# Performance work log

Measured on AMD Instinct MI355X. Metric: run time of the kernel, lower is better.

Reference implementation:

```python
import jax, jax.numpy as jnp
import numpy as np

H = 16
D_MODEL = 1024
D_K = D_MODEL // H


def setup_inputs() -> dict:
    key = jax.random.key(0)
    ks = jax.random.split(key, 11)
    B, S = 4, 2048
    scale = 1.0 / np.sqrt(D_MODEL)
    inp = {
        "query": jax.random.normal(ks[0], (B, S, D_MODEL), dtype=jnp.float32),
        "key": jax.random.normal(ks[1], (B, S, D_MODEL), dtype=jnp.float32),
        "value": jax.random.normal(ks[2], (B, S, D_MODEL), dtype=jnp.float32),
        "Wq": jax.random.normal(ks[3], (D_MODEL, D_MODEL), dtype=jnp.float32) * scale,
        "bq": jnp.zeros((D_MODEL,), dtype=jnp.float32),
        "Wk": jax.random.normal(ks[4], (D_MODEL, D_MODEL), dtype=jnp.float32) * scale,
        "bk": jnp.zeros((D_MODEL,), dtype=jnp.float32),
        "Wv": jax.random.normal(ks[5], (D_MODEL, D_MODEL), dtype=jnp.float32) * scale,
        "bv": jnp.zeros((D_MODEL,), dtype=jnp.float32),
        "Wo": jax.random.normal(ks[6], (D_MODEL, D_MODEL), dtype=jnp.float32) * scale,
        "bo": jnp.zeros((D_MODEL,), dtype=jnp.float32),
    }
    return inp


def reference(query, key, value, Wq, bq, Wk, bk, Wv, bv, Wo, bo):
    B, S, _ = query.shape

    def proj(x, W, b):
        # nn.Linear: x @ W.T + b, then split heads -> [B, H, S, D_K]
        y = jnp.einsum("bsd,ed->bse", x, W) + b
        return y.reshape(B, S, H, D_K).transpose(0, 2, 1, 3)

    q = proj(query, Wq, bq)
    k = proj(key, Wk, bk)
    v = proj(value, Wv, bv)

    scores = jnp.einsum("bhqd,bhkd->bhqk", q, k) / jnp.sqrt(jnp.float32(D_K))
    attn = jax.nn.softmax(scores, axis=-1)
    out = jnp.einsum("bhqk,bhkd->bhqd", attn, v)  # [B,H,S,D_K]
    out = out.transpose(0, 2, 1, 3).reshape(B, S, H * D_K)
    # final linear (dropout disabled in eval / deterministic reference)
    return jnp.einsum("bsd,ed->bse", out, Wo) + bo
```

## Files before the change

### kernel.cpp

```cpp
#include <hip/hip_runtime.h>
#include <stdint.h>

typedef __attribute__((ext_vector_type(8))) short short8;
typedef __attribute__((ext_vector_type(4))) float floatx4;

#define DEV __device__ __forceinline__

DEV unsigned short f2bf(float x) {
  unsigned u = __float_as_uint(x);
  u += 0x7fffu + ((u >> 16) & 1u);
  return (unsigned short)(u >> 16);
}

DEV unsigned pkbf(float hi, float lo) {
  return __builtin_amdgcn_perm(__float_as_uint(hi) + 0x8000u,
                               __float_as_uint(lo) + 0x8000u, 0x07060302u);
}

DEV void load_lds16(const unsigned short* g, unsigned short* l) {
  __builtin_amdgcn_global_load_lds(
      (const __attribute__((address_space(1))) void*)g,
      (__attribute__((address_space(3))) void*)l, 16, 0, 0);
}

DEV void lds_fence() { asm volatile("" ::: "memory"); }

__global__ void cvt_all(const float* __restrict__ Wq, const float* __restrict__ Wk,
                        const float* __restrict__ Wv, const float* __restrict__ Wo,
                        const float* __restrict__ Xq, const float* __restrict__ Xk,
                        const float* __restrict__ Xv,
                        unsigned short* __restrict__ Wb, unsigned short* __restrict__ XqB,
                        unsigned short* __restrict__ XkB, unsigned short* __restrict__ XvB) {
  int bid = blockIdx.x;
  const float* src;
  unsigned short* dst;
  int off;
  if (bid < 4096) {
    int sel = bid >> 10;
    src = sel == 0 ? Wq : sel == 1 ? Wk : sel == 2 ? Wv : Wo;
    dst = Wb + (size_t)sel * 1048576;
    off = bid & 1023;
  } else {
    bid -= 4096;
    int sel = bid >> 13;
    src = sel == 0 ? Xq : sel == 1 ? Xk : Xv;
    dst = sel == 0 ? XqB : sel == 1 ? XkB : XvB;
    off = bid & 8191;
  }
  int i = (off * 256 + threadIdx.x) * 4;
  float4 v = *(const float4*)(src + i);
  uint2 o;
  o.x = pkbf(v.y, v.x);
  o.y = pkbf(v.w, v.z);
  *(uint2*)(dst + i) = o;
}

#define SCQ (0.125f * 1.44269504089f)
__global__ __launch_bounds__(256, 2) void qkv_gemm(
    const unsigned short* __restrict__ XqB, const unsigned short* __restrict__ XkB,
    const unsigned short* __restrict__ XvB,
    const unsigned short* __restrict__ Wb,
    const float* __restrict__ bq, const float* __restrict__ bk, const float* __restrict__ bv,
    unsigned short* __restrict__ Qp, unsigned short* __restrict__ Kp,
    unsigned short* __restrict__ VTp) {
  __shared__ alignas(16) unsigned short Xs[2][128 * 32];
  __shared__ alignas(16) unsigned short Ws[2][128 * 32];
  const int z = blockIdx.z;
  const unsigned short* X = z == 0 ? XqB : z == 1 ? XkB : XvB;
  const unsigned short* W = Wb + (size_t)z * 1048576;
  const float* bias = z == 0 ? bq : z == 1 ? bk : bv;

  const int tid = threadIdx.x;
  const int lane = tid & 63, wave = tid >> 6;
  const int lcol = lane & 15, quad = lane >> 4;
  const int wo = blockIdx.x * 128;
  const int xo = blockIdx.y * 128;
  const int wm = (wave & 1) * 64;
  const int wn = (wave >> 1) * 64;

  floatx4 acc[4][4];
  for (int mi = 0; mi < 4; ++mi)
    for (int ni = 0; ni < 4; ++ni)
      for (int r = 0; r < 4; ++r) acc[mi][ni][r] = 0.f;

  {
    int c = tid;
    load_lds16(W + (size_t)(wo + (c >> 2)) * 1024 + (c & 3) * 8, Ws[0] + c * 8);
    load_lds16(X + (size_t)(xo + (c >> 2)) * 1024 + (c & 3) * 8, Xs[0] + c * 8);
    c = tid + 256;
    load_lds16(W + (size_t)(wo + (c >> 2)) * 1024 + (c & 3) * 8, Ws[0] + c * 8);
    load_lds16(X + (size_t)(xo + (c >> 2)) * 1024 + (c & 3) * 8, Xs[0] + c * 8);
  }
  __syncthreads();

  for (int kt = 0; kt < 32; ++kt) {
    const int cur = kt & 1;
    if (kt != 31) {
      const int k0 = (kt + 1) * 32;
      int c = tid;
      load_lds16(W + (size_t)(wo + (c >> 2)) * 1024 + k0 + (c & 3) * 8, Ws[cur ^ 1] + c * 8);
      load_lds16(X + (size_t)(xo + (c >> 2)) * 1024 + k0 + (c & 3) * 8, Xs[cur ^ 1] + c * 8);
      c = tid + 256;
      load_lds16(W + (size_t)(wo + (c >> 2)) * 1024 + k0 + (c & 3) * 8, Ws[cur ^ 1] + c * 8);
      load_lds16(X + (size_t)(xo + (c >> 2)) * 1024 + k0 + (c & 3) * 8, Xs[cur ^ 1] + c * 8);
    }
    const unsigned short* Ab = (z < 2) ? Xs[cur] : Ws[cur];
    const unsigned short* Bb = (z < 2) ? Ws[cur] : Xs[cur];
    short8 af[4], bfr[4];
#pragma unroll
    for (int mi = 0; mi < 4; ++mi)
      af[mi] = *(const short8*)(Ab + (wm + mi * 16 + lcol) * 32 + quad * 8);
#pragma unroll
    for (int ni = 0; ni < 4; ++ni)
      bfr[ni] = *(const short8*)(Bb + (wn + ni * 16 + lcol) * 32 + quad * 8);
#pragma unroll
    for (int mi = 0; mi < 4; ++mi)
#pragma unroll
      for (int ni = 0; ni < 4; ++ni)
        acc[mi][ni] = __builtin_amdgcn_mfma_f32_16x16x32_bf16(af[mi], bfr[ni], acc[mi][ni], 0, 0, 0);
    __syncthreads();
  }

  if (z < 2) {
    unsigned short* Out = z == 0 ? Qp : Kp;
    const float scl = z == 0 ? SCQ : 1.f;
#pragma unroll
    for (int ni = 0; ni < 4; ++ni) {
      int col = wo + wn + ni * 16 + lcol;
      float bvx = bias[col];
      int h = col >> 6, d = col & 63;
#pragma unroll
      for (int mi = 0; mi < 4; ++mi) {
        int rbase = xo + wm + mi * 16 + quad * 4;
#pragma unroll
        for (int r = 0; r < 4; ++r) {
          int grow = rbase + r;
          int bb = grow >> 11, s = grow & 2047;
          Out[((size_t)(bb * 16 + h) * 2048 + s) * 64 + d] = f2bf((acc[mi][ni][r] + bvx) * scl);
        }
      }
    }
  } else {
#pragma unroll
    for (int mi = 0; mi < 4; ++mi) {
      int dbase = wo + wm + mi * 16 + quad * 4;
#pragma unroll
      for (int r = 0; r < 4; ++r) {
        int dg = dbase + r;
        float bvx = bias[dg];
        int h = dg >> 6, dk = dg & 63;
#pragma unroll
        for (int ni = 0; ni < 4; ++ni) {
          int sg = xo + wn + ni * 16 + lcol;
          int bb = sg >> 11, ss = sg & 2047;
          VTp[((size_t)(bb * 16 + h) * 64 + dk) * 2048 + ss] = f2bf(acc[mi][ni][r] + bvx);
        }
      }
    }
  }
}

__global__ __launch_bounds__(256, 2) void gemm_o(
    const unsigned short* __restrict__ A, const unsigned short* __restrict__ Bw,
    const float* __restrict__ bias, float* __restrict__ Out) {
  __shared__ alignas(16) unsigned short As[2][128 * 32];
  __shared__ alignas(16) unsigned short Bs[2][128 * 32];
  const int tid = threadIdx.x;
  const int lane = tid & 63, wave = tid >> 6;
  const int lcol = lane & 15, quad = lane >> 4;
  const int n0 = blockIdx.x * 128;
  const int m0 = blockIdx.y * 128;
  const int wm = (wave & 1) * 64;
  const int wn = (wave >> 1) * 64;

  floatx4 acc[4][4];
  for (int mi = 0; mi < 4; ++mi)
    for (int ni = 0; ni < 4; ++ni)
      for (int r = 0; r < 4; ++r) acc[mi][ni][r] = 0.f;

  {
    int c = tid;
    load_lds16(Bw + (size_t)(n0 + (c >> 2)) * 1024 + (c & 3) * 8, Bs[0] + c * 8);
    load_lds16(A  + (size_t)(m0 + (c >> 2)) * 1024 + (c & 3) * 8, As[0] + c * 8);
    c = tid + 256;
    load_lds16(Bw + (size_t)(n0 + (c >> 2)) * 1024 + (c & 3) * 8, Bs[0] + c * 8);
    load_lds16(A  + (size_t)(m0 + (c >> 2)) * 1024 + (c & 3) * 8, As[0] + c * 8);
  }
  __syncthreads();

  for (int kt = 0; kt < 32; ++kt) {
    const int cur = kt & 1;
    if (kt != 31) {
      const int k0 = (kt + 1) * 32;
      int c = tid;
      load_lds16(Bw + (size_t)(n0 + (c >> 2)) * 1024 + k0 + (c & 3) * 8, Bs[cur ^ 1] + c * 8);
      load_lds16(A  + (size_t)(m0 + (c >> 2)) * 1024 + k0 + (c & 3) * 8, As[cur ^ 1] + c * 8);
      c = tid + 256;
      load_lds16(Bw + (size_t)(n0 + (c >> 2)) * 1024 + k0 + (c & 3) * 8, Bs[cur ^ 1] + c * 8);
      load_lds16(A  + (size_t)(m0 + (c >> 2)) * 1024 + k0 + (c & 3) * 8, As[cur ^ 1] + c * 8);
    }
    short8 af[4], bfr[4];
#pragma unroll
    for (int mi = 0; mi < 4; ++mi)
      af[mi] = *(const short8*)(As[cur] + (wm + mi * 16 + lcol) * 32 + quad * 8);
#pragma unroll
    for (int ni = 0; ni < 4; ++ni)
      bfr[ni] = *(const short8*)(Bs[cur] + (wn + ni * 16 + lcol) * 32 + quad * 8);
#pragma unroll
    for (int mi = 0; mi < 4; ++mi)
#pragma unroll
      for (int ni = 0; ni < 4; ++ni)
        acc[mi][ni] = __builtin_amdgcn_mfma_f32_16x16x32_bf16(af[mi], bfr[ni], acc[mi][ni], 0, 0, 0);
    __syncthreads();
  }
#pragma unroll
  for (int ni = 0; ni < 4; ++ni) {
    int col = n0 + wn + ni * 16 + lcol;
    float bv = bias[col];
#pragma unroll
    for (int mi = 0; mi < 4; ++mi) {
      int rbase = m0 + wm + mi * 16 + quad * 4;
#pragma unroll
      for (int r = 0; r < 4; ++r)
        Out[(size_t)(rbase + r) * 1024 + col] = acc[mi][ni][r] + bv;
    }
  }
}

__global__ __launch_bounds__(256, 2) void attn_kernel(
    const unsigned short* __restrict__ Qp, const unsigned short* __restrict__ Kp,
    const unsigned short* __restrict__ VTp, unsigned short* __restrict__ Ctx) {
  __shared__ alignas(16) unsigned short Ks[2][128 * 64];
  __shared__ alignas(16) unsigned short Vt[2][64 * 128];
  __shared__ alignas(16) unsigned short Ps[128 * 64];

  const int tid = threadIdx.x;
  const int lane = tid & 63, wave = tid >> 6;
  const int lcol = lane & 15, quad = lane >> 4;
  const int wq = wave * 32;
  const int qt = blockIdx.x, h = blockIdx.y, b = blockIdx.z;
  const size_t bh = (size_t)(b * 16 + h) * 2048 * 64;
  const unsigned short* Qb = Qp + bh + (size_t)qt * 128 * 64;
  const unsigned short* Kb = Kp + bh;
  const unsigned short* VTb = VTp + (size_t)(b * 16 + h) * 64 * 2048;

#pragma unroll
  for (int i = 0; i < 4; ++i) {
    int p = tid + i * 256;
    int row = p >> 3, pj = p & 7;
    load_lds16(Qb + row * 64 + ((pj ^ (row & 7)) * 8), Ps + p * 8);
  }
#pragma unroll
  for (int i = 0; i < 4; ++i) {
    int p = tid + i * 256;
    int kr = p >> 3, kj = p & 7;
    load_lds16(Kb + kr * 64 + ((kj ^ (kr & 7)) * 8), Ks[0] + p * 8);
    int vr = p >> 4, vj = p & 15;
    load_lds16(VTb + (size_t)vr * 2048 + ((vj ^ (vr & 7)) * 8), Vt[0] + p * 8);
  }
  __syncthreads();

  short8 qf[2][2];
#pragma unroll
  for (int ni = 0; ni < 2; ++ni)
#pragma unroll
    for (int ks = 0; ks < 2; ++ks) {
      int row = wq + ni * 16 + lcol;
      qf[ni][ks] = *(const short8*)(Ps + row * 64 + (((ks * 4 + quad) ^ (row & 7)) * 8));
    }

  float M[2] = {-1e30f, -1e30f};
  float L[2] = {0.f, 0.f};
  floatx4 Oacc[2][4];
  for (int mi = 0; mi < 2; ++mi)
    for (int nd = 0; nd < 4; ++nd)
      for (int r = 0; r < 4; ++r) Oacc[mi][nd][r] = 0.f;

  for (int jt = 0; jt < 16; ++jt) {
    const int cur = jt & 1;
    if (jt != 15) {
#pragma unroll
      for (int i = 0; i < 4; ++i) {
        int p = tid + i * 256;
        int kr = p >> 3, kj = p & 7;
        load_lds16(Kb + (size_t)(jt + 1) * 8192 + kr * 64 + ((kj ^ (kr & 7)) * 8),
                   Ks[cur ^ 1] + p * 8);
        int vr = p >> 4, vj = p & 15;
        load_lds16(VTb + (size_t)vr * 2048 + (jt + 1) * 128 + ((vj ^ (vr & 7)) * 8),
                   Vt[cur ^ 1] + p * 8);
      }
    }

    const unsigned short* Kc = Ks[cur];
    floatx4 sacc[8][2];
    for (int mi = 0; mi < 8; ++mi)
      for (int ni = 0; ni < 2; ++ni)
        for (int r = 0; r < 4; ++r) sacc[mi][ni][r] = 0.f;
#pragma unroll
    for (int mi = 0; mi < 8; ++mi) {
      int row = mi * 16 + lcol;
      int sw = (row & 7);
      short8 kf0 = *(const short8*)(Kc + row * 64 + ((quad ^ sw) * 8));
      short8 kf1 = *(const short8*)(Kc + row * 64 + (((4 + quad) ^ sw) * 8));
#pragma unroll
      for (int ni = 0; ni < 2; ++ni) {
        sacc[mi][ni] = __builtin_amdgcn_mfma_f32_16x16x32_bf16(kf0, qf[ni][0], sacc[mi][ni], 0, 0, 0);
        sacc[mi][ni] = __builtin_amdgcn_mfma_f32_16x16x32_bf16(kf1, qf[ni][1], sacc[mi][ni], 0, 0, 0);
      }
    }

    float mx[2];
#pragma unroll
    for (int ni = 0; ni < 2; ++ni) {
      float pm[8];
#pragma unroll
      for (int mi = 0; mi < 8; ++mi)
        pm[mi] = fmaxf(fmaxf(sacc[mi][ni][0], sacc[mi][ni][1]),
                       fmaxf(sacc[mi][ni][2], sacc[mi][ni][3]));
      float t0 = fmaxf(fmaxf(pm[0], pm[1]), fmaxf(pm[2], pm[3]));
      float t1 = fmaxf(fmaxf(pm[4], pm[5]), fmaxf(pm[6], pm[7]));
      float m = fmaxf(t0, t1);
      m = fmaxf(m, __shfl_xor(m, 16));
      m = fmaxf(m, __shfl_xor(m, 32));
      mx[ni] = m;
    }
    const int skip = __all((mx[0] <= M[0] + 8.f) & (mx[1] <= M[1] + 8.f));
    float alpha[2] = {1.f, 1.f};
    if (!skip) {
#pragma unroll
      for (int ni = 0; ni < 2; ++ni) {
        float mnew = fmaxf(M[ni], mx[ni]);
        alpha[ni] = exp2f(M[ni] - mnew);
        M[ni] = mnew;
      }
#pragma unroll
      for (int mi = 0; mi < 2; ++mi)
#pragma unroll
        for (int r = 0; r < 4; ++r) {
          float a = __shfl(alpha[mi], quad * 4 + r);
          floatx4 av = {a, a, a, a};
#pragma unroll
          for (int nd = 0; nd < 4; ++nd) Oacc[mi][nd] *= av;
        }
    }
#pragma unroll
    for (int ni = 0; ni < 2; ++ni) {
      floatx4 mv = {M[ni], M[ni], M[ni], M[ni]};
      floatx4 rv = {0.f, 0.f, 0.f, 0.f};
#pragma unroll
      for (int mi = 0; mi < 8; ++mi) {
        floatx4 t = sacc[mi][ni] - mv;
        floatx4 p;
        p[0] = exp2f(t[0]); p[1] = exp2f(t[1]); p[2] = exp2f(t[2]); p[3] = exp2f(t[3]);
        sacc[mi][ni] = p;
        rv += p;
      }
      float rs = (rv[0] + rv[1]) + (rv[2] + rv[3]);
      rs += __shfl_xor(rs, 16);
      rs += __shfl_xor(rs, 32);
      L[ni] = skip ? (L[ni] + rs) : (L[ni] * alpha[ni] + rs);
    }

    const unsigned short* Vc = Vt[cur];
#pragma unroll
    for (int half = 0; half < 2; ++half) {
#pragma unroll
      for (int ni = 0; ni < 2; ++ni) {
        int q = wq + ni * 16 + lcol;
        int sw = q & 7;
#pragma unroll
        for (int m2 = 0; m2 < 4; ++m2) {
          int mi = half * 4 + m2;
          uint2 pw;
          pw.x = pkbf(sacc[mi][ni][1], sacc[mi][ni][0]);
          pw.y = pkbf(sacc[mi][ni][3], sacc[mi][ni][2]);
          int j = 2 * m2 + (quad >> 1);
          *(uint2*)(Ps + q * 64 + ((j ^ sw) * 8) + (quad & 1) * 4) = pw;
        }
      }
      lds_fence();
#pragma unroll
      for (int kk = 0; kk < 2; ++kk) {
        short8 pf[2];
#pragma unroll
        for (int mi = 0; mi < 2; ++mi) {
          int q = wq + mi * 16 + lcol;
          pf[mi] = *(const short8*)(Ps + q * 64 + (((4 * kk + quad) ^ (q & 7)) * 8));
        }
#pragma unroll
        for (int nd = 0; nd < 4; ++nd) {
          int d = nd * 16 + lcol;
          short8 vf = *(const short8*)(Vc + d * 128 + ((((half * 2 + kk) * 4 + quad) ^ (d & 7)) * 8));
#pragma unroll
          for (int mi = 0; mi < 2; ++mi)
            Oacc[mi][nd] = __builtin_amdgcn_mfma_f32_16x16x32_bf16(pf[mi], vf, Oacc[mi][nd], 0, 0, 0);
        }
      }
      lds_fence();
    }
    __syncthreads();
  }

  float linv[2] = {1.f / L[0], 1.f / L[1]};
#pragma unroll
  for (int mi = 0; mi < 2; ++mi)
#pragma unroll
    for (int r = 0; r < 4; ++r) {
      float li = __shfl(linv[mi], quad * 4 + r);
      int q = wq + mi * 16 + quad * 4 + r;
      int sw = q & 7;
#pragma unroll
      for (int nd = 0; nd < 4; ++nd) {
        int j = 2 * nd + (lcol >> 3);
        Ps[q * 64 + ((j ^ sw) * 8) + (lcol & 7)] = f2bf(Oacc[mi][nd][r] * li);
      }
    }
  __syncthreads();
#pragma unroll
  for (int i = 0; i < 4; ++i) {
    int c = tid + i * 256;
    int row = c >> 3, pj = c & 7;
    uint4 v = *(const uint4*)(Ps + row * 64 + ((pj ^ (row & 7)) * 8));
    *(uint4*)(Ctx + ((size_t)(b * 2048 + qt * 128 + row)) * 1024 + h * 64 + pj * 8) = v;
  }
}

extern "C" void kernel_launch(void* const* d_in, const int* in_sizes, int n_in,
                              void* d_out, int out_size, void* d_ws, size_t ws_size,
                              hipStream_t stream) {
  const float* query = (const float*)d_in[0];
  const float* key_  = (const float*)d_in[1];
  const float* value = (const float*)d_in[2];
  const float* Wq = (const float*)d_in[3];
  const float* bq = (const float*)d_in[4];
  const float* Wk = (const float*)d_in[5];
  const float* bk = (const float*)d_in[6];
  const float* Wv = (const float*)d_in[7];
  const float* bv = (const float*)d_in[8];
  const float* Wo = (const float*)d_in[9];
  const float* bo = (const float*)d_in[10];

  char* w = (char*)d_ws;
  unsigned short* Wb  = (unsigned short*)w; w += (size_t)4 * 1024 * 1024 * 2;
  unsigned short* Qp  = (unsigned short*)w; w += (size_t)8192 * 1024 * 2;
  unsigned short* Kp  = (unsigned short*)w; w += (size_t)8192 * 1024 * 2;
  unsigned short* VTp = (unsigned short*)w; w += (size_t)8192 * 1024 * 2;
  unsigned short* Ctx = (unsigned short*)w; w += (size_t)8192 * 1024 * 2;

  unsigned short* XqB = (unsigned short*)d_out;
  unsigned short* XkB = (unsigned short*)d_out + (size_t)8192 * 1024;
  unsigned short* XvB = Ctx;

  cvt_all<<<28672, 256, 0, stream>>>(Wq, Wk, Wv, Wo, query, key_, value,
                                     Wb, XqB, XkB, XvB);

  qkv_gemm<<<dim3(8, 64, 3), 256, 0, stream>>>(XqB, XkB, XvB, Wb,
                                               bq, bk, bv, Qp, Kp, VTp);

  attn_kernel<<<dim3(16, 16, 4), 256, 0, stream>>>(Qp, Kp, VTp, Ctx);

  gemm_o<<<dim3(8, 64), 256, 0, stream>>>(Ctx, Wb + (size_t)3 * 1048576, bo, (float*)d_out);
}
```

Measured before the change: 414.2 us.

## Triple-buffer GEMM pipelines, vectorize epilogues, shrink attention KV tile for occupancy

```diff
diff --git a/kernel.cpp b/kernel.cpp
--- a/kernel.cpp
+++ b/kernel.cpp
@@ -24,6 +24,9 @@
 }
 
 DEV void lds_fence() { asm volatile("" ::: "memory"); }
+
+#define ASM_VMCNT(n) asm volatile("s_waitcnt vmcnt(" #n ")" ::: "memory")
+DEV void sched_fence() { __builtin_amdgcn_sched_barrier(0); }
 
 __global__ void cvt_all(const float* __restrict__ Wq, const float* __restrict__ Wk,
                         const float* __restrict__ Wv, const float* __restrict__ Wo,
@@ -56,15 +59,15 @@
 }
 
 #define SCQ (0.125f * 1.44269504089f)
-__global__ __launch_bounds__(256, 2) void qkv_gemm(
+__global__ __launch_bounds__(256, 3) void qkv_gemm(
     const unsigned short* __restrict__ XqB, const unsigned short* __restrict__ XkB,
     const unsigned short* __restrict__ XvB,
     const unsigned short* __restrict__ Wb,
     const float* __restrict__ bq, const float* __restrict__ bk, const float* __restrict__ bv,
     unsigned short* __restrict__ Qp, unsigned short* __restrict__ Kp,
     unsigned short* __restrict__ VTp) {
-  __shared__ alignas(16) unsigned short Xs[2][128 * 32];
-  __shared__ alignas(16) unsigned short Ws[2][128 * 32];
+  __shared__ alignas(16) unsigned short Xs[3][128 * 32];
+  __shared__ alignas(16) unsigned short Ws[3][128 * 32];
   const int z = blockIdx.z;
   const unsigned short* X = z == 0 ? XqB : z == 1 ? XkB : XvB;
   const unsigned short* W = Wb + (size_t)z * 1048576;
@@ -83,29 +86,28 @@
     for (int ni = 0; ni < 4; ++ni)
       for (int r = 0; r < 4; ++r) acc[mi][ni][r] = 0.f;
 
-  {
+  auto stage = [&](int kt, int buf) {
+    const int k0 = kt * 32;
     int c = tid;
-    load_lds16(W + (size_t)(wo + (c >> 2)) * 1024 + (c & 3) * 8, Ws[0] + c * 8);
-    load_lds16(X + (size_t)(xo + (c >> 2)) * 1024 + (c & 3) * 8, Xs[0] + c * 8);
+    load_lds16(W + (size_t)(wo + (c >> 2)) * 1024 + k0 + (c & 3) * 8, Ws[buf] + c * 8);
+    load_lds16(X + (size_t)(xo + (c >> 2)) * 1024 + k0 + (c & 3) * 8, Xs[buf] + c * 8);
     c = tid + 256;
-    load_lds16(W + (size_t)(wo + (c >> 2)) * 1024 + (c & 3) * 8, Ws[0] + c * 8);
-    load_lds16(X + (size_t)(xo + (c >> 2)) * 1024 + (c & 3) * 8, Xs[0] + c * 8);
-  }
-  __syncthreads();
-
+    load_lds16(W + (size_t)(wo + (c >> 2)) * 1024 + k0 + (c & 3) * 8, Ws[buf] + c * 8);
+    load_lds16(X + (size_t)(xo + (c >> 2)) * 1024 + k0 + (c & 3) * 8, Xs[buf] + c * 8);
+  };
+
+  stage(0, 0);
+  stage(1, 1);
+  int cur = 0;
   for (int kt = 0; kt < 32; ++kt) {
-    const int cur = kt & 1;
-    if (kt != 31) {
-      const int k0 = (kt + 1) * 32;
-      int c = tid;
-      load_lds16(W + (size_t)(wo + (c >> 2)) * 1024 + k0 + (c & 3) * 8, Ws[cur ^ 1] + c * 8);
-      load_lds16(X + (size_t)(xo + (c >> 2)) * 1024 + k0 + (c & 3) * 8, Xs[cur ^ 1] + c * 8);
-      c = tid + 256;
-      load_lds16(W + (size_t)(wo + (c >> 2)) * 1024 + k0 + (c & 3) * 8, Ws[cur ^ 1] + c * 8);
-      load_lds16(X + (size_t)(xo + (c >> 2)) * 1024 + k0 + (c & 3) * 8, Xs[cur ^ 1] + c * 8);
-    }
-    const unsigned short* Ab = (z < 2) ? Xs[cur] : Ws[cur];
-    const unsigned short* Bb = (z < 2) ? Ws[cur] : Xs[cur];
+    sched_fence();
+    ASM_VMCNT(4);
+    __builtin_amdgcn_s_barrier();
+    sched_fence();
+    int nb = cur + 2; if (nb >= 3) nb -= 3;
+    stage((kt + 2) & 31, nb);
+    const unsigned short* Ab = (z < 2) ? Ws[cur] : Xs[cur];
+    const unsigned short* Bb = (z < 2) ? Xs[cur] : Ws[cur];
     short8 af[4], bfr[4];
 #pragma unroll
     for (int mi = 0; mi < 4; ++mi)
@@ -118,58 +120,56 @@
 #pragma unroll
       for (int ni = 0; ni < 4; ++ni)
         acc[mi][ni] = __builtin_amdgcn_mfma_f32_16x16x32_bf16(af[mi], bfr[ni], acc[mi][ni], 0, 0, 0);
-    __syncthreads();
+    cur = (cur == 2) ? 0 : cur + 1;
   }
 
   if (z < 2) {
     unsigned short* Out = z == 0 ? Qp : Kp;
     const float scl = z == 0 ? SCQ : 1.f;
 #pragma unroll
-    for (int ni = 0; ni < 4; ++ni) {
-      int col = wo + wn + ni * 16 + lcol;
-      float bvx = bias[col];
-      int h = col >> 6, d = col & 63;
-#pragma unroll
-      for (int mi = 0; mi < 4; ++mi) {
-        int rbase = xo + wm + mi * 16 + quad * 4;
-#pragma unroll
-        for (int r = 0; r < 4; ++r) {
-          int grow = rbase + r;
-          int bb = grow >> 11, s = grow & 2047;
-          Out[((size_t)(bb * 16 + h) * 2048 + s) * 64 + d] = f2bf((acc[mi][ni][r] + bvx) * scl);
-        }
-      }
-    }
-  } else {
-#pragma unroll
     for (int mi = 0; mi < 4; ++mi) {
       int dbase = wo + wm + mi * 16 + quad * 4;
-#pragma unroll
-      for (int r = 0; r < 4; ++r) {
-        int dg = dbase + r;
-        float bvx = bias[dg];
-        int h = dg >> 6, dk = dg & 63;
-#pragma unroll
-        for (int ni = 0; ni < 4; ++ni) {
-          int sg = xo + wn + ni * 16 + lcol;
-          int bb = sg >> 11, ss = sg & 2047;
-          VTp[((size_t)(bb * 16 + h) * 64 + dk) * 2048 + ss] = f2bf(acc[mi][ni][r] + bvx);
-        }
-      }
-    }
-  }
-}
-
-__global__ __launch_bounds__(256, 2) void gemm_o(
+      float4 bv4 = *(const float4*)(bias + dbase);
+      int h = dbase >> 6, dk = dbase & 63;
+#pragma unroll
+      for (int ni = 0; ni < 4; ++ni) {
+        int sg = xo + wn + ni * 16 + lcol;
+        int bb = sg >> 11, ss = sg & 2047;
+        uint2 o;
+        o.x = pkbf((acc[mi][ni][1] + bv4.y) * scl, (acc[mi][ni][0] + bv4.x) * scl);
+        o.y = pkbf((acc[mi][ni][3] + bv4.w) * scl, (acc[mi][ni][2] + bv4.z) * scl);
+        *(uint2*)(Out + ((size_t)(bb * 16 + h) * 2048 + ss) * 64 + dk) = o;
+      }
+    }
+  } else {
+#pragma unroll
+    for (int ni = 0; ni < 4; ++ni) {
+      int dg = wo + wn + ni * 16 + lcol;
+      float bvx = bias[dg];
+      int h = dg >> 6, dk = dg & 63;
+#pragma unroll
+      for (int mi = 0; mi < 4; ++mi) {
+        int sbase = xo + wm + mi * 16 + quad * 4;
+        int bb = sbase >> 11, ss = sbase & 2047;
+        uint2 o;
+        o.x = pkbf(acc[mi][ni][1] + bvx, acc[mi][ni][0] + bvx);
+        o.y = pkbf(acc[mi][ni][3] + bvx, acc[mi][ni][2] + bvx);
+        *(uint2*)(VTp + ((size_t)(bb * 16 + h) * 64 + dk) * 2048 + ss) = o;
+      }
+    }
+  }
+}
+
+__global__ __launch_bounds__(256, 3) void gemm_o(
     const unsigned short* __restrict__ A, const unsigned short* __restrict__ Bw,
     const float* __restrict__ bias, float* __restrict__ Out) {
-  __shared__ alignas(16) unsigned short As[2][128 * 32];
-  __shared__ alignas(16) unsigned short Bs[2][128 * 32];
+  __shared__ alignas(16) unsigned short Cs[3][128 * 32];
+  __shared__ alignas(16) unsigned short Wos[3][128 * 32];
   const int tid = threadIdx.x;
   const int lane = tid & 63, wave = tid >> 6;
   const int lcol = lane & 15, quad = lane >> 4;
-  const int n0 = blockIdx.x * 128;
-  const int m0 = blockIdx.y * 128;
+  const int co = blockIdx.x * 128;
+  const int so = blockIdx.y * 128;
   const int wm = (wave & 1) * 64;
   const int wn = (wave >> 1) * 64;
 
@@ -178,60 +178,62 @@
     for (int ni = 0; ni < 4; ++ni)
       for (int r = 0; r < 4; ++r) acc[mi][ni][r] = 0.f;
 
-  {
+  auto stage = [&](int kt, int buf) {
+    const int k0 = kt * 32;
     int c = tid;
-    load_lds16(Bw + (size_t)(n0 + (c >> 2)) * 1024 + (c & 3) * 8, Bs[0] + c * 8);
-    load_lds16(A  + (size_t)(m0 + (c >> 2)) * 1024 + (c & 3) * 8, As[0] + c * 8);
+    load_lds16(Bw + (size_t)(co + (c >> 2)) * 1024 + k0 + (c & 3) * 8, Wos[buf] + c * 8);
+    load_lds16(A  + (size_t)(so + (c >> 2)) * 1024 + k0 + (c & 3) * 8, Cs[buf] + c * 8);
     c = tid + 256;
-    load_lds16(Bw + (size_t)(n0 + (c >> 2)) * 1024 + (c & 3) * 8, Bs[0] + c * 8);
-    load_lds16(A  + (size_t)(m0 + (c >> 2)) * 1024 + (c & 3) * 8, As[0] + c * 8);
-  }
-  __syncthreads();
-
+    load_lds16(Bw + (size_t)(co + (c >> 2)) * 1024 + k0 + (c & 3) * 8, Wos[buf] + c * 8);
+    load_lds16(A  + (size_t)(so + (c >> 2)) * 1024 + k0 + (c & 3) * 8, Cs[buf] + c * 8);
+  };
+
+  stage(0, 0);
+  stage(1, 1);
+  int cur = 0;
   for (int kt = 0; kt < 32; ++kt) {
-    const int cur = kt & 1;
-    if (kt != 31) {
-      const int k0 = (kt + 1) * 32;
-      int c = tid;
-      load_lds16(Bw + (size_t)(n0 + (c >> 2)) * 1024 + k0 + (c & 3) * 8, Bs[cur ^ 1] + c * 8);
-      load_lds16(A  + (size_t)(m0 + (c >> 2)) * 1024 + k0 + (c & 3) * 8, As[cur ^ 1] + c * 8);
-      c = tid + 256;
-      load_lds16(Bw + (size_t)(n0 + (c >> 2)) * 1024 + k0 + (c & 3) * 8, Bs[cur ^ 1] + c * 8);
-      load_lds16(A  + (size_t)(m0 + (c >> 2)) * 1024 + k0 + (c & 3) * 8, As[cur ^ 1] + c * 8);
-    }
+    sched_fence();
+    ASM_VMCNT(4);
+    __builtin_amdgcn_s_barrier();
+    sched_fence();
+    int nb = cur + 2; if (nb >= 3) nb -= 3;
+    stage((kt + 2) & 31, nb);
     short8 af[4], bfr[4];
 #pragma unroll
     for (int mi = 0; mi < 4; ++mi)
-      af[mi] = *(const short8*)(As[cur] + (wm + mi * 16 + lcol) * 32 + quad * 8);
+      af[mi] = *(const short8*)(Wos[cur] + (wm + mi * 16 + lcol) * 32 + quad * 8);
 #pragma unroll
     for (int ni = 0; ni < 4; ++ni)
-      bfr[ni] = *(const short8*)(Bs[cur] + (wn + ni * 16 + lcol) * 32 + quad * 8);
+      bfr[ni] = *(const short8*)(Cs[cur] + (wn + ni * 16 + lcol) * 32 + quad * 8);
 #pragma unroll
     for (int mi = 0; mi < 4; ++mi)
 #pragma unroll
       for (int ni = 0; ni < 4; ++ni)
         acc[mi][ni] = __builtin_amdgcn_mfma_f32_16x16x32_bf16(af[mi], bfr[ni], acc[mi][ni], 0, 0, 0);
-    __syncthreads();
-  }
-#pragma unroll
-  for (int ni = 0; ni < 4; ++ni) {
-    int col = n0 + wn + ni * 16 + lcol;
-    float bv = bias[col];
-#pragma unroll
-    for (int mi = 0; mi < 4; ++mi) {
-      int rbase = m0 + wm + mi * 16 + quad * 4;
-#pragma unroll
-      for (int r = 0; r < 4; ++r)
-        Out[(size_t)(rbase + r) * 1024 + col] = acc[mi][ni][r] + bv;
-    }
-  }
-}
-
-__global__ __launch_bounds__(256, 2) void attn_kernel(
+    cur = (cur == 2) ? 0 : cur + 1;
+  }
+#pragma unroll
+  for (int mi = 0; mi < 4; ++mi) {
+    int cb = co + wm + mi * 16 + quad * 4;
+    float4 bv4 = *(const float4*)(bias + cb);
+#pragma unroll
+    for (int ni = 0; ni < 4; ++ni) {
+      int sg = so + wn + ni * 16 + lcol;
+      float4 o;
+      o.x = acc[mi][ni][0] + bv4.x;
+      o.y = acc[mi][ni][1] + bv4.y;
+      o.z = acc[mi][ni][2] + bv4.z;
+      o.w = acc[mi][ni][3] + bv4.w;
+      *(float4*)(Out + (size_t)sg * 1024 + cb) = o;
+    }
+  }
+}
+
+__global__ __launch_bounds__(256, 4) void attn_kernel(
     const unsigned short* __restrict__ Qp, const unsigned short* __restrict__ Kp,
     const unsigned short* __restrict__ VTp, unsigned short* __restrict__ Ctx) {
-  __shared__ alignas(16) unsigned short Ks[2][128 * 64];
-  __shared__ alignas(16) unsigned short Vt[2][64 * 128];
+  __shared__ alignas(16) unsigned short Ks[2][64 * 64];
+  __shared__ alignas(16) unsigned short Vt[64 * 64];
   __shared__ alignas(16) unsigned short Ps[128 * 64];
 
   const int tid = threadIdx.x;
@@ -251,12 +253,10 @@
     load_lds16(Qb + row * 64 + ((pj ^ (row & 7)) * 8), Ps + p * 8);
   }
 #pragma unroll
-  for (int i = 0; i < 4; ++i) {
+  for (int i = 0; i < 2; ++i) {
     int p = tid + i * 256;
     int kr = p >> 3, kj = p & 7;
     load_lds16(Kb + kr * 64 + ((kj ^ (kr & 7)) * 8), Ks[0] + p * 8);
-    int vr = p >> 4, vj = p & 15;
-    load_lds16(VTb + (size_t)vr * 2048 + ((vj ^ (vr & 7)) * 8), Vt[0] + p * 8);
   }
   __syncthreads();
 
@@ -276,28 +276,29 @@
     for (int nd = 0; nd < 4; ++nd)
       for (int r = 0; r < 4; ++r) Oacc[mi][nd][r] = 0.f;
 
-  for (int jt = 0; jt < 16; ++jt) {
+  for (int jt = 0; jt < 32; ++jt) {
     const int cur = jt & 1;
-    if (jt != 15) {
-#pragma unroll
-      for (int i = 0; i < 4; ++i) {
-        int p = tid + i * 256;
-        int kr = p >> 3, kj = p & 7;
-        load_lds16(Kb + (size_t)(jt + 1) * 8192 + kr * 64 + ((kj ^ (kr & 7)) * 8),
-                   Ks[cur ^ 1] + p * 8);
-        int vr = p >> 4, vj = p & 15;
-        load_lds16(VTb + (size_t)vr * 2048 + (jt + 1) * 128 + ((vj ^ (vr & 7)) * 8),
-                   Vt[cur ^ 1] + p * 8);
-      }
+#pragma unroll
+    for (int i = 0; i < 2; ++i) {
+      int p = tid + i * 256;
+      int vr = p >> 3, vj = p & 7;
+      load_lds16(VTb + (size_t)vr * 2048 + jt * 64 + ((vj ^ (vr & 7)) * 8), Vt + p * 8);
+    }
+    const int jn = (jt + 1) & 31;
+#pragma unroll
+    for (int i = 0; i < 2; ++i) {
+      int p = tid + i * 256;
+      int kr = p >> 3, kj = p & 7;
+      load_lds16(Kb + (size_t)jn * 4096 + kr * 64 + ((kj ^ (kr & 7)) * 8), Ks[cur ^ 1] + p * 8);
     }
 
     const unsigned short* Kc = Ks[cur];
-    floatx4 sacc[8][2];
-    for (int mi = 0; mi < 8; ++mi)
+    floatx4 sacc[4][2];
+    for (int mi = 0; mi < 4; ++mi)
       for (int ni = 0; ni < 2; ++ni)
         for (int r = 0; r < 4; ++r) sacc[mi][ni][r] = 0.f;
 #pragma unroll
-    for (int mi = 0; mi < 8; ++mi) {
+    for (int mi = 0; mi < 4; ++mi) {
       int row = mi * 16 + lcol;
       int sw = (row & 7);
       short8 kf0 = *(const short8*)(Kc + row * 64 + ((quad ^ sw) * 8));
@@ -312,14 +313,12 @@
     float mx[2];
 #pragma unroll
     for (int ni = 0; ni < 2; ++ni) {
-      float pm[8];
-#pragma unroll
-      for (int mi = 0; mi < 8; ++mi)
+      float pm[4];
+#pragma unroll
+      for (int mi = 0; mi < 4; ++mi)
         pm[mi] = fmaxf(fmaxf(sacc[mi][ni][0], sacc[mi][ni][1]),
                        fmaxf(sacc[mi][ni][2], sacc[mi][ni][3]));
-      float t0 = fmaxf(fmaxf(pm[0], pm[1]), fmaxf(pm[2], pm[3]));
-      float t1 = fmaxf(fmaxf(pm[4], pm[5]), fmaxf(pm[6], pm[7]));
-      float m = fmaxf(t0, t1);
+      float m = fmaxf(fmaxf(pm[0], pm[1]), fmaxf(pm[2], pm[3]));
       m = fmaxf(m, __shfl_xor(m, 16));
       m = fmaxf(m, __shfl_xor(m, 32));
       mx[ni] = m;
@@ -348,7 +347,7 @@
       floatx4 mv = {M[ni], M[ni], M[ni], M[ni]};
       floatx4 rv = {0.f, 0.f, 0.f, 0.f};
 #pragma unroll
-      for (int mi = 0; mi < 8; ++mi) {
+      for (int mi = 0; mi < 4; ++mi) {
         floatx4 t = sacc[mi][ni] - mv;
         floatx4 p;
         p[0] = exp2f(t[0]); p[1] = exp2f(t[1]); p[2] = exp2f(t[2]); p[3] = exp2f(t[3]);
@@ -361,43 +360,44 @@
       L[ni] = skip ? (L[ni] + rs) : (L[ni] * alpha[ni] + rs);
     }
 
-    const unsigned short* Vc = Vt[cur];
-#pragma unroll
-    for (int half = 0; half < 2; ++half) {
-#pragma unroll
-      for (int ni = 0; ni < 2; ++ni) {
-        int q = wq + ni * 16 + lcol;
-        int sw = q & 7;
-#pragma unroll
-        for (int m2 = 0; m2 < 4; ++m2) {
-          int mi = half * 4 + m2;
-          uint2 pw;
-          pw.x = pkbf(sacc[mi][ni][1], sacc[mi][ni][0]);
-          pw.y = pkbf(sacc[mi][ni][3], sacc[mi][ni][2]);
-          int j = 2 * m2 + (quad >> 1);
-          *(uint2*)(Ps + q * 64 + ((j ^ sw) * 8) + (quad & 1) * 4) = pw;
-        }
-      }
-      lds_fence();
-#pragma unroll
-      for (int kk = 0; kk < 2; ++kk) {
-        short8 pf[2];
-#pragma unroll
-        for (int mi = 0; mi < 2; ++mi) {
-          int q = wq + mi * 16 + lcol;
-          pf[mi] = *(const short8*)(Ps + q * 64 + (((4 * kk + quad) ^ (q & 7)) * 8));
-        }
-#pragma unroll
-        for (int nd = 0; nd < 4; ++nd) {
-          int d = nd * 16 + lcol;
-          short8 vf = *(const short8*)(Vc + d * 128 + ((((half * 2 + kk) * 4 + quad) ^ (d & 7)) * 8));
-#pragma unroll
-          for (int mi = 0; mi < 2; ++mi)
-            Oacc[mi][nd] = __builtin_amdgcn_mfma_f32_16x16x32_bf16(pf[mi], vf, Oacc[mi][nd], 0, 0, 0);
-        }
-      }
-      lds_fence();
-    }
+#pragma unroll
+    for (int ni = 0; ni < 2; ++ni) {
+      int q = wq + ni * 16 + lcol;
+      int sw = q & 7;
+#pragma unroll
+      for (int mi = 0; mi < 4; ++mi) {
+        uint2 pw;
+        pw.x = pkbf(sacc[mi][ni][1], sacc[mi][ni][0]);
+        pw.y = pkbf(sacc[mi][ni][3], sacc[mi][ni][2]);
+        int j = 2 * mi + (quad >> 1);
+        *(uint2*)(Ps + q * 64 + ((j ^ sw) * 8) + (quad & 1) * 4) = pw;
+      }
+    }
+    lds_fence();
+
+    sched_fence();
+    ASM_VMCNT(2);
+    __builtin_amdgcn_s_barrier();
+    sched_fence();
+
+#pragma unroll
+    for (int kk = 0; kk < 2; ++kk) {
+      short8 pf[2];
+#pragma unroll
+      for (int mi = 0; mi < 2; ++mi) {
+        int q = wq + mi * 16 + lcol;
+        pf[mi] = *(const short8*)(Ps + q * 64 + (((kk * 4 + quad) ^ (q & 7)) * 8));
+      }
+#pragma unroll
+      for (int nd = 0; nd < 4; ++nd) {
+        int d = nd * 16 + lcol;
+        short8 vf = *(const short8*)(Vt + d * 64 + (((kk * 4 + quad) ^ (d & 7)) * 8));
+#pragma unroll
+        for (int mi = 0; mi < 2; ++mi)
+          Oacc[mi][nd] = __builtin_amdgcn_mfma_f32_16x16x32_bf16(pf[mi], vf, Oacc[mi][nd], 0, 0, 0);
+      }
+    }
+    lds_fence();
     __syncthreads();
   }
 
```

After: 400.8 us. -3.2%, faster.
